# Kernel optimization log

Hardware: AMD Instinct MI355X
Metric: run time of the kernel (lower is better)

The kernel has to match this reference:

```python
import jax, jax.numpy as jnp
import numpy as np

B, N, IN_DIM, D, H, L = 8, 256, 2, 128, 512, 2
EPS = 1e-5


def layer_norm(x, g, b):
    m = jnp.mean(x, axis=-1, keepdims=True)
    v = jnp.var(x, axis=-1, keepdims=True)
    return (x - m) * jax.lax.rsqrt(v + EPS) * g + b


def loo_max_pool(nodes):
    # nodes: (B, N, D) -> leave-one-out max over the set axis -> (B, N, D)
    n = nodes.shape[1]
    neg = jnp.finfo(nodes.dtype).min
    mask = jnp.eye(n, dtype=bool)[None, :, :, None]          # (1, N, N, 1)
    expanded = jnp.broadcast_to(nodes[:, None, :, :],
                                (nodes.shape[0], n, n, nodes.shape[2]))
    return jnp.where(mask, neg, expanded).max(axis=2)        # (B, N, D)


def setup_inputs() -> dict:
    key = jax.random.key(0)
    ks = jax.random.split(key, 16)
    s = 0.02
    inp = {
        "x":   jax.random.normal(ks[0], (B, N, IN_DIM), dtype=jnp.float32),
        # embedding linear + its LayerNorm
        "We":  jax.random.normal(ks[1], (IN_DIM, D)) * s,
        "be":  jnp.zeros((D,), jnp.float32),
        "ge":  jnp.ones((D,), jnp.float32),
        "bge": jnp.zeros((D,), jnp.float32),
        # per-layer pool linear (concat of x and LOO-pooled context: 2D -> D)
        "Wp":  jax.random.normal(ks[2], (L, 2 * D, D)) * s,
        "bp":  jnp.zeros((L, D), jnp.float32),
        "gp":  jnp.ones((L, D), jnp.float32),
        "bgp": jnp.zeros((L, D), jnp.float32),
        # per-layer feed-forward D -> H -> D
        "W1":  jax.random.normal(ks[3], (L, D, H)) * s,
        "b1":  jnp.zeros((L, H), jnp.float32),
        "W2":  jax.random.normal(ks[4], (L, H, D)) * s,
        "b2":  jnp.zeros((L, D), jnp.float32),
        "gf":  jnp.ones((L, D), jnp.float32),
        "bgf": jnp.zeros((L, D), jnp.float32),
    }
    return inp


def reference(x, We, be, ge, bge, Wp, bp, gp, bgp, W1, b1, W2, b2, gf, bgf):
    # embeddings + embedding norm
    h = layer_norm(x @ We + be, ge, bge)                      # (B, N, D)
    for i in range(L):
        # pool layer: LOO max pooling, concat, linear, residual, norm
        pooled = loo_max_pool(h)                              # (B, N, D)
        cat = jnp.concatenate([h, pooled], axis=-1)           # (B, N, 2D)
        h = layer_norm(h + cat @ Wp[i] + bp[i], gp[i], bgp[i])
        # feed-forward, residual, norm
        ff = jax.nn.relu(h @ W1[i] + b1[i]) @ W2[i] + b2[i]
        h = layer_norm(h + ff, gf[i], bgf[i])
    return h
```

## Files before the change

kernel.cpp:

```cpp
#include <hip/hip_runtime.h>
#include <hip/hip_bf16.h>

#define BB 8
#define NN 256
#define DD 128
#define HH 512
#define LL 2
#define EPSV 1e-5f
#define TPB 8
#define BPL (NN/TPB)

typedef unsigned short ushort_t;
typedef __attribute__((ext_vector_type(8))) short bf16x8;
typedef __attribute__((ext_vector_type(4))) float f32x4;

#define WPSZ (256*128)
#define W1SZ (128*512)
#define W2SZ (512*128)
#define LAYSZ (WPSZ+W1SZ+W2SZ)
#define TOTW (2*LAYSZ)

#if defined(__has_builtin)
#if __has_builtin(__builtin_amdgcn_sched_barrier)
#define SCHED_FENCE() __builtin_amdgcn_sched_barrier(0)
#endif
#endif
#ifndef SCHED_FENCE
#define SCHED_FENCE()
#endif

__device__ __forceinline__ ushort_t f2b(float v){
  __hip_bfloat16 h = __float2bfloat16(v);
  return *(ushort_t*)&h;
}

__device__ __forceinline__ void waveRed2(float &a, float &b){
  #pragma unroll
  for (int off=32; off>=1; off>>=1){
    a += __shfl_xor(a, off, 64);
    b += __shfl_xor(b, off, 64);
  }
}

__device__ __forceinline__ void poolMerge(float &m1, float &m2, int &am,
                                          float o1, float o2, int oa){
  if (o1 > m1){ m2 = fmaxf(m1, o2); m1 = o1; am = oa; }
  else        { m2 = fmaxf(m2, o1); }
}

__global__ __launch_bounds__(512) void k_prep(
    const float* __restrict__ Wp, const float* __restrict__ W1,
    const float* __restrict__ W2, ushort_t* __restrict__ wcvt)
{
  int e8 = blockIdx.x*512 + threadIdx.x;
  if (e8 >= TOTW/8) return;
  int e = e8*8;
  int l2 = (e >= LAYSZ) ? 1 : 0;
  int el = e - l2*LAYSZ;
  const float* src; int N, KSlog, off;
  if (el < WPSZ)           { src = Wp + (size_t)l2*WPSZ; N = 128; KSlog = 3; off = el; }
  else if (el < WPSZ+W1SZ) { src = W1 + (size_t)l2*W1SZ; N = 512; KSlog = 2; off = el - WPSZ; }
  else                     { src = W2 + (size_t)l2*W2SZ; N = 128; KSlog = 4; off = el - (WPSZ+W1SZ); }
  int rec  = off >> 9;
  int ln   = (off >> 3) & 63;
  int n0t  = rec >> KSlog;
  int ks   = rec & ((1<<KSlog)-1);
  int row0 = ks*32 + ((ln>>4)<<3);
  int col  = (n0t<<4) + (ln&15);
  bf16x8 v;
  #pragma unroll
  for (int j=0;j<8;++j) v[j] = (short)f2b(src[(size_t)(row0+j)*N + col]);
  *(bf16x8*)(wcvt + e) = v;
}

__global__ __launch_bounds__(512, 2) void k_net(
    int layer,
    const float* __restrict__ x, const float* __restrict__ We,
    const float* __restrict__ be, const float* __restrict__ ge,
    const float* __restrict__ bge,
    float* __restrict__ hio,
    float* __restrict__ pm1, float* __restrict__ pm2, int* __restrict__ pma,
    const ushort_t* __restrict__ wL,
    const float* __restrict__ bp,
    const float* __restrict__ gp, const float* __restrict__ bgp,
    const float* __restrict__ b1,
    const float* __restrict__ b2,
    const float* __restrict__ gf, const float* __restrict__ bgf)
{
  int tid = threadIdx.x;
  int d = tid & 127, fourth = tid >> 7;
  int wv = tid >> 6;
  int lane = tid & 63;
  int m = lane & 15, q = lane >> 4;
  int t0 = blockIdx.x * TPB;
  int b = t0 >> 8;
  int blk = (t0 >> 3) & (BPL-1);
  int n0a = wv*16;

  const ushort_t* wAb = wL;
  const ushort_t* wBb = wL + WPSZ;
  const ushort_t* wCb = wL + WPSZ + W1SZ;

  bf16x8 wfa[8], wfb[16];
  #pragma unroll
  for (int ks=0; ks<8; ++ks)
    wfa[ks] = *(const bf16x8*)(wAb + ((size_t)(wv*8+ks)*64 + lane)*8);
  #pragma unroll
  for (int r=0; r<16; ++r)
    wfb[r] = *(const bf16x8*)(wBb + ((size_t)(((r>>2)*8+wv)*4 + (r&3))*64 + lane)*8);
  SCHED_FENCE();

  __shared__ float    hcur[8*128];
  __shared__ ushort_t catb[16*256];
  __shared__ float    sA[16*128];
  __shared__ ushort_t h1b[16*128];
  __shared__ float    h1f[8*128];
  __shared__ ushort_t ub[16*512];
  __shared__ float fm1[128], fm2[128];
  __shared__ int   fam[128];
  __shared__ float sm1[4][128], sm2[4][128];
  __shared__ int   sam[4][128];
  __shared__ float xs[512];
  __shared__ float red9[2][12];
  __shared__ float stats[12];
  __shared__ float4 tk[256];

  if (layer == 0){
    xs[tid] = x[(size_t)b*512 + tid];
    float a = We[d], bw = We[128+d], c = be[d];
    if (fourth == 0){
      float r0=a, r1=bw;        waveRed2(r0,r1);
      float r2=c, r3=a*a;       waveRed2(r2,r3);
      float r4=bw*bw, r5=c*c;   waveRed2(r4,r5);
      float r6=a*bw, r7=a*c;    waveRed2(r6,r7);
      float r8=bw*c, r9=0.f;    waveRed2(r8,r9);
      int w = (tid >> 6) & 1;
      if (lane == 0){
        red9[w][0]=r0; red9[w][1]=r1; red9[w][2]=r2; red9[w][3]=r3;
        red9[w][4]=r4; red9[w][5]=r5; red9[w][6]=r6; red9[w][7]=r7;
        red9[w][8]=r8;
      }
    }
    __syncthreads();
    if (tid < 9) stats[tid] = (red9[0][tid] + red9[1][tid]) * (1.f/128);
    __syncthreads();
    if (tid < 256){
      float mA=stats[0], mB=stats[1], mC=stats[2];
      float SAA=stats[3], SBB=stats[4], SCC=stats[5];
      float SAB=stats[6], SAC=stats[7], SBC=stats[8];
      float x0 = xs[2*tid], x1 = xs[2*tid+1];
      float mean = fmaf(x0, mA, fmaf(x1, mB, mC));
      float ev2  = x0*x0*SAA + x1*x1*SBB + SCC
                 + 2.f*(x0*x1*SAB + x0*SAC + x1*SBC);
      float var = ev2 - mean*mean;
      tk[tid] = make_float4(x0, x1, mean, rsqrtf(var + EPSV));
    }
    __syncthreads();
    float gev = ge[d], bgev = bge[d];
    float m1=-3.4e38f, m2=-3.4e38f; int am=0;
    for (int i=0;i<64;++i){
      int n = fourth*64 + i;
      float4 t4 = tk[n];
      float v  = fmaf(t4.x, a, fmaf(t4.y, bw, c));
      float hv = fmaf((v - t4.z)*t4.w, gev, bgev);
      poolMerge(m1,m2,am, hv, -3.4e38f, n);
    }
    sm1[fourth][d]=m1; sm2[fourth][d]=m2; sam[fourth][d]=am;
    #pragma unroll
    for (int rep=0; rep<2; ++rep){
      int t = fourth*2 + rep;
      int n = (t0 & 255) + t;
      float4 t4 = tk[n];
      float v  = fmaf(t4.x, a, fmaf(t4.y, bw, c));
      float hv = fmaf((v - t4.z)*t4.w, gev, bgev);
      hcur[t*128 + d] = hv;
      *(ushort_t*)((char*)catb + (((t*256 + d)*2) ^ ((t&7)<<4))) = f2b(hv);
    }
    __syncthreads();
  } else {
    {
      size_t base = ((size_t)b*BPL + fourth*8)*128 + d;
      float m1 = pm1[base], m2 = pm2[base]; int am = pma[base];
      #pragma unroll
      for (int i=1;i<8;++i)
        poolMerge(m1,m2,am, pm1[base+(size_t)i*128], pm2[base+(size_t)i*128],
                  pma[base+(size_t)i*128]);
      sm1[fourth][d]=m1; sm2[fourth][d]=m2; sam[fourth][d]=am;
    }
    #pragma unroll
    for (int rep=0; rep<2; ++rep){
      int t = fourth*2 + rep;
      float hv = hio[(size_t)(t0+t)*DD + d];
      hcur[t*128 + d] = hv;
      *(ushort_t*)((char*)catb + (((t*256 + d)*2) ^ ((t&7)<<4))) = f2b(hv);
    }
    __syncthreads();
  }

  if (fourth==0){
    float m1=sm1[0][d], m2=sm2[0][d]; int am=sam[0][d];
    #pragma unroll
    for (int p=1;p<4;++p) poolMerge(m1,m2,am, sm1[p][d], sm2[p][d], sam[p][d]);
    fm1[d]=m1; fm2[d]=m2; fam[d]=am;
  }
  __syncthreads();

  #pragma unroll
  for (int rep=0; rep<2; ++rep){
    int e = rep*512 + tid;
    int t = e >> 7, c2 = e & 127;
    int n = (t0 & 255) + t;
    float v = (n==fam[c2]) ? fm2[c2] : fm1[c2];
    *(ushort_t*)((char*)catb + (((t*256 + 128 + c2)*2) ^ ((t&7)<<4))) = f2b(v);
  }
  __syncthreads();

  {
    f32x4 acc = {0.f,0.f,0.f,0.f};
    const char* apb = (const char*)catb;
    int abase = (m*256 + q*8)*2;
    int sw = (m&7)<<4;
    #pragma unroll
    for (int ks=0; ks<8; ++ks){
      bf16x8 af = *(const bf16x8*)(apb + ((abase + ks*64) ^ sw));
      acc = __builtin_amdgcn_mfma_f32_16x16x32_bf16(af, wfa[ks], acc, 0,0,0);
    }
    #pragma unroll
    for (int r=0;r<4;++r) sA[(q*4+r)*128 + n0a + m] = acc[r];
  }
  bf16x8 wfc[16];
  #pragma unroll
  for (int kk=0; kk<16; ++kk)
    wfc[kk] = *(const bf16x8*)(wCb + ((size_t)(wv*16+kk)*64 + lane)*8);
  SCHED_FENCE();
  __syncthreads();

  {
    int t = wv, g = lane;
    float2 v2 = *(const float2*)&sA[t*128 + 2*g];
    float v0 = v2.x + bp[2*g]   + hcur[t*128 + 2*g];
    float v1 = v2.y + bp[2*g+1] + hcur[t*128 + 2*g + 1];
    float s = v0+v1, qq = v0*v0 + v1*v1;
    waveRed2(s,qq);
    float mean = s*(1.f/128), var = qq*(1.f/128) - mean*mean;
    float rs = rsqrtf(var + EPSV);
    float o0 = (v0-mean)*rs*gp[2*g]   + bgp[2*g];
    float o1 = (v1-mean)*rs*gp[2*g+1] + bgp[2*g+1];
    unsigned pk = (unsigned)f2b(o0) | ((unsigned)f2b(o1) << 16);
    *(unsigned*)((char*)h1b + (((t*128 + 2*g)*2) ^ ((t&7)<<4))) = pk;
    *(float2*)&h1f[t*128 + 2*g] = make_float2(o0, o1);
  }
  __syncthreads();

  {
    const char* apb = (const char*)h1b;
    int abase = (m*128 + q*8)*2;
    int sw = (m&7)<<4;
    bf16x8 af[4];
    #pragma unroll
    for (int ks=0; ks<4; ++ks)
      af[ks] = *(const bf16x8*)(apb + ((abase + ks*64) ^ sw));
    #pragma unroll
    for (int half=0; half<2; ++half){
      #pragma unroll
      for (int i=0;i<2;++i){
        int idx4 = half*2+i;
        int n0 = idx4*128 + wv*16;
        f32x4 acc = {0.f,0.f,0.f,0.f};
        #pragma unroll
        for (int ks=0; ks<4; ++ks)
          acc = __builtin_amdgcn_mfma_f32_16x16x32_bf16(af[ks], wfb[idx4*4+ks], acc, 0,0,0);
        float bb = b1[n0+m];
        #pragma unroll
        for (int r=0;r<4;++r){
          int row = q*4+r;
          *(ushort_t*)((char*)ub + (((row*512 + n0 + m)*2) ^ ((row&7)<<4)))
              = f2b(fmaxf(acc[r] + bb, 0.f));
        }
      }
    }
  }
  __syncthreads();

  {
    f32x4 acc = {0.f,0.f,0.f,0.f};
    const char* apb = (const char*)ub;
    int abase = (m*512 + q*8)*2;
    int sw = (m&7)<<4;
    #pragma unroll
    for (int kk=0; kk<16; ++kk){
      bf16x8 af = *(const bf16x8*)(apb + ((abase + kk*64) ^ sw));
      acc = __builtin_amdgcn_mfma_f32_16x16x32_bf16(af, wfc[kk], acc, 0,0,0);
    }
    #pragma unroll
    for (int r=0;r<4;++r) sA[(q*4+r)*128 + n0a + m] = acc[r];
  }
  __syncthreads();

  {
    int t = wv, g = lane;
    float2 v2 = *(const float2*)&sA[t*128 + 2*g];
    float v0 = v2.x + b2[2*g]   + h1f[t*128 + 2*g];
    float v1 = v2.y + b2[2*g+1] + h1f[t*128 + 2*g + 1];
    float s = v0+v1, qq = v0*v0 + v1*v1;
    waveRed2(s,qq);
    float mean = s*(1.f/128), var = qq*(1.f/128) - mean*mean;
    float rs = rsqrtf(var + EPSV);
    float o0 = (v0-mean)*rs*gf[2*g]   + bgf[2*g];
    float o1 = (v1-mean)*rs*gf[2*g+1] + bgf[2*g+1];
    *(float2*)&hio[(size_t)(t0+t)*DD + 2*g] = make_float2(o0, o1);
    *(float2*)&hcur[t*128 + 2*g] = make_float2(o0, o1);
  }
  if (layer == 0){
    __syncthreads();
    if (tid < 128){
      int n0 = t0 & 255;
      float m1 = hcur[tid], m2 = -3.4e38f; int am = n0;
      #pragma unroll
      for (int p=1;p<TPB;++p)
        poolMerge(m1,m2,am, hcur[p*128+tid], -3.4e38f, n0+p);
      size_t idx = ((size_t)b*BPL + blk)*128 + tid;
      pm1[idx]=m1; pm2[idx]=m2; pma[idx]=am;
    }
  }
}

extern "C" void kernel_launch(void* const* d_in, const int* in_sizes, int n_in,
                              void* d_out, int out_size, void* d_ws, size_t ws_size,
                              hipStream_t stream)
{
  const float* x   = (const float*)d_in[0];
  const float* We  = (const float*)d_in[1];
  const float* be  = (const float*)d_in[2];
  const float* ge  = (const float*)d_in[3];
  const float* bge = (const float*)d_in[4];
  const float* Wp  = (const float*)d_in[5];
  const float* bp  = (const float*)d_in[6];
  const float* gp  = (const float*)d_in[7];
  const float* bgp = (const float*)d_in[8];
  const float* W1  = (const float*)d_in[9];
  const float* b1  = (const float*)d_in[10];
  const float* W2  = (const float*)d_in[11];
  const float* b2  = (const float*)d_in[12];
  const float* gf  = (const float*)d_in[13];
  const float* bgf = (const float*)d_in[14];

  float* hio = (float*)d_out;
  char* ws = (char*)d_ws;
  const size_t NP = (size_t)BB*BPL*128;
  float* p1 = (float*)ws;            ws += NP*4;
  float* p2 = (float*)ws;            ws += NP*4;
  int*   pa = (int*)ws;              ws += NP*4;
  ushort_t* wcvt = (ushort_t*)ws;

  const int grid = (BB*NN)/TPB;

  k_prep<<<80, 512, 0, stream>>>(Wp, W1, W2, wcvt);

  k_net<<<grid, 512, 0, stream>>>(0, x, We, be, ge, bge, hio, p1, p2, pa,
      wcvt,
      bp,      gp,      bgp,
      b1,      b2,
      gf,      bgf);

  k_net<<<grid, 512, 0, stream>>>(1, x, We, be, ge, bge, hio, p1, p2, pa,
      wcvt + LAYSZ,
      bp + DD, gp + DD, bgp + DD,
      b1 + HH, b2 + DD,
      gf + DD, bgf + DD);
}
```

Baseline: 103.6 us.

## Hoist embedding LayerNorm and pooled max stats into prep kernel

Before this change, each of the 256 layer-0 blocks recomputed the embedding LayerNorm for all 256 set elements of its batch so it could find the leave-one-out max statistics. Now 8 extra blocks in the prep kernel compute h0 and the per-batch top-2 and argmax once, and write them to workspace. Layer-0 blocks just read their rows and the stats. This removes redundant per-block compute and shared memory, at the cost of a global round trip for h0 (1 MB) and a serial dependency on the prep kernel.

```diff
diff --git a/kernel.cpp b/kernel.cpp
--- a/kernel.cpp
+++ b/kernel.cpp
@@ -19,6 +19,7 @@
 #define W2SZ (512*128)
 #define LAYSZ (WPSZ+W1SZ+W2SZ)
 #define TOTW (2*LAYSZ)
+#define WBLK 80
 
 #if defined(__has_builtin)
 #if __has_builtin(__builtin_amdgcn_sched_barrier)
@@ -50,37 +51,104 @@
 
 __global__ __launch_bounds__(512) void k_prep(
     const float* __restrict__ Wp, const float* __restrict__ W1,
-    const float* __restrict__ W2, ushort_t* __restrict__ wcvt)
-{
-  int e8 = blockIdx.x*512 + threadIdx.x;
-  if (e8 >= TOTW/8) return;
-  int e = e8*8;
-  int l2 = (e >= LAYSZ) ? 1 : 0;
-  int el = e - l2*LAYSZ;
-  const float* src; int N, KSlog, off;
-  if (el < WPSZ)           { src = Wp + (size_t)l2*WPSZ; N = 128; KSlog = 3; off = el; }
-  else if (el < WPSZ+W1SZ) { src = W1 + (size_t)l2*W1SZ; N = 512; KSlog = 2; off = el - WPSZ; }
-  else                     { src = W2 + (size_t)l2*W2SZ; N = 128; KSlog = 4; off = el - (WPSZ+W1SZ); }
-  int rec  = off >> 9;
-  int ln   = (off >> 3) & 63;
-  int n0t  = rec >> KSlog;
-  int ks   = rec & ((1<<KSlog)-1);
-  int row0 = ks*32 + ((ln>>4)<<3);
-  int col  = (n0t<<4) + (ln&15);
-  bf16x8 v;
-  #pragma unroll
-  for (int j=0;j<8;++j) v[j] = (short)f2b(src[(size_t)(row0+j)*N + col]);
-  *(bf16x8*)(wcvt + e) = v;
-}
-
-__global__ __launch_bounds__(512, 2) void k_net(
-    int layer,
+    const float* __restrict__ W2,
     const float* __restrict__ x, const float* __restrict__ We,
     const float* __restrict__ be, const float* __restrict__ ge,
     const float* __restrict__ bge,
+    ushort_t* __restrict__ wcvt, float* __restrict__ h0w,
+    float* __restrict__ fm1w, float* __restrict__ fm2w,
+    int* __restrict__ famw)
+{
+  int tid = threadIdx.x;
+  if (blockIdx.x < WBLK){
+    int e8 = blockIdx.x*512 + tid;
+    int e = e8*8;
+    int l2 = (e >= LAYSZ) ? 1 : 0;
+    int el = e - l2*LAYSZ;
+    const float* src; int N, KSlog, off;
+    if (el < WPSZ)           { src = Wp + (size_t)l2*WPSZ; N = 128; KSlog = 3; off = el; }
+    else if (el < WPSZ+W1SZ) { src = W1 + (size_t)l2*W1SZ; N = 512; KSlog = 2; off = el - WPSZ; }
+    else                     { src = W2 + (size_t)l2*W2SZ; N = 128; KSlog = 4; off = el - (WPSZ+W1SZ); }
+    int rec  = off >> 9;
+    int ln   = (off >> 3) & 63;
+    int n0t  = rec >> KSlog;
+    int ks   = rec & ((1<<KSlog)-1);
+    int row0 = ks*32 + ((ln>>4)<<3);
+    int col  = (n0t<<4) + (ln&15);
+    bf16x8 v;
+    #pragma unroll
+    for (int j=0;j<8;++j) v[j] = (short)f2b(src[(size_t)(row0+j)*N + col]);
+    *(bf16x8*)(wcvt + e) = v;
+    return;
+  }
+
+  int bb = blockIdx.x - WBLK;
+  int d = tid & 127, fourth = tid >> 7, lane = tid & 63;
+
+  __shared__ float xs[512];
+  __shared__ float red9[2][12];
+  __shared__ float stats[12];
+  __shared__ float4 tk[256];
+  __shared__ float sm1[4][128], sm2[4][128];
+  __shared__ int   sam[4][128];
+
+  xs[tid] = x[(size_t)bb*512 + tid];
+  float a = We[d], bw = We[128+d], c = be[d];
+  if (fourth == 0){
+    float r0=a, r1=bw;        waveRed2(r0,r1);
+    float r2=c, r3=a*a;       waveRed2(r2,r3);
+    float r4=bw*bw, r5=c*c;   waveRed2(r4,r5);
+    float r6=a*bw, r7=a*c;    waveRed2(r6,r7);
+    float r8=bw*c, r9=0.f;    waveRed2(r8,r9);
+    int w = (tid >> 6) & 1;
+    if (lane == 0){
+      red9[w][0]=r0; red9[w][1]=r1; red9[w][2]=r2; red9[w][3]=r3;
+      red9[w][4]=r4; red9[w][5]=r5; red9[w][6]=r6; red9[w][7]=r7;
+      red9[w][8]=r8;
+    }
+  }
+  __syncthreads();
+  if (tid < 9) stats[tid] = (red9[0][tid] + red9[1][tid]) * (1.f/128);
+  __syncthreads();
+  if (tid < 256){
+    float mA=stats[0], mB=stats[1], mC=stats[2];
+    float SAA=stats[3], SBB=stats[4], SCC=stats[5];
+    float SAB=stats[6], SAC=stats[7], SBC=stats[8];
+    float x0 = xs[2*tid], x1 = xs[2*tid+1];
+    float mean = fmaf(x0, mA, fmaf(x1, mB, mC));
+    float ev2  = x0*x0*SAA + x1*x1*SBB + SCC
+               + 2.f*(x0*x1*SAB + x0*SAC + x1*SBC);
+    float var = ev2 - mean*mean;
+    tk[tid] = make_float4(x0, x1, mean, rsqrtf(var + EPSV));
+  }
+  __syncthreads();
+  float gev = ge[d], bgev = bge[d];
+  float m1=-3.4e38f, m2=-3.4e38f; int am=0;
+  for (int i=0;i<64;++i){
+    int n = fourth*64 + i;
+    float4 t4 = tk[n];
+    float v  = fmaf(t4.x, a, fmaf(t4.y, bw, c));
+    float hv = fmaf((v - t4.z)*t4.w, gev, bgev);
+    h0w[((size_t)bb*256 + n)*128 + d] = hv;
+    poolMerge(m1,m2,am, hv, -3.4e38f, n);
+  }
+  sm1[fourth][d]=m1; sm2[fourth][d]=m2; sam[fourth][d]=am;
+  __syncthreads();
+  if (fourth==0){
+    float M1=sm1[0][d], M2=sm2[0][d]; int AM=sam[0][d];
+    #pragma unroll
+    for (int p=1;p<4;++p) poolMerge(M1,M2,AM, sm1[p][d], sm2[p][d], sam[p][d]);
+    fm1w[bb*128+d]=M1; fm2w[bb*128+d]=M2; famw[bb*128+d]=AM;
+  }
+}
+
+__global__ __launch_bounds__(512, 2) void k_net(
+    int layer,
     float* __restrict__ hio,
     float* __restrict__ pm1, float* __restrict__ pm2, int* __restrict__ pma,
     const ushort_t* __restrict__ wL,
+    const float* __restrict__ h0w, const float* __restrict__ fm1w,
+    const float* __restrict__ fm2w, const int* __restrict__ famw,
     const float* __restrict__ bp,
     const float* __restrict__ gp, const float* __restrict__ bgp,
     const float* __restrict__ b1,
@@ -120,61 +188,28 @@
   __shared__ int   fam[128];
   __shared__ float sm1[4][128], sm2[4][128];
   __shared__ int   sam[4][128];
-  __shared__ float xs[512];
-  __shared__ float red9[2][12];
-  __shared__ float stats[12];
-  __shared__ float4 tk[256];
 
   if (layer == 0){
-    xs[tid] = x[(size_t)b*512 + tid];
-    float a = We[d], bw = We[128+d], c = be[d];
-    if (fourth == 0){
-      float r0=a, r1=bw;        waveRed2(r0,r1);
-      float r2=c, r3=a*a;       waveRed2(r2,r3);
-      float r4=bw*bw, r5=c*c;   waveRed2(r4,r5);
-      float r6=a*bw, r7=a*c;    waveRed2(r6,r7);
-      float r8=bw*c, r9=0.f;    waveRed2(r8,r9);
-      int w = (tid >> 6) & 1;
-      if (lane == 0){
-        red9[w][0]=r0; red9[w][1]=r1; red9[w][2]=r2; red9[w][3]=r3;
-        red9[w][4]=r4; red9[w][5]=r5; red9[w][6]=r6; red9[w][7]=r7;
-        red9[w][8]=r8;
-      }
-    }
-    __syncthreads();
-    if (tid < 9) stats[tid] = (red9[0][tid] + red9[1][tid]) * (1.f/128);
-    __syncthreads();
-    if (tid < 256){
-      float mA=stats[0], mB=stats[1], mC=stats[2];
-      float SAA=stats[3], SBB=stats[4], SCC=stats[5];
-      float SAB=stats[6], SAC=stats[7], SBC=stats[8];
-      float x0 = xs[2*tid], x1 = xs[2*tid+1];
-      float mean = fmaf(x0, mA, fmaf(x1, mB, mC));
-      float ev2  = x0*x0*SAA + x1*x1*SBB + SCC
-                 + 2.f*(x0*x1*SAB + x0*SAC + x1*SBC);
-      float var = ev2 - mean*mean;
-      tk[tid] = make_float4(x0, x1, mean, rsqrtf(var + EPSV));
-    }
-    __syncthreads();
-    float gev = ge[d], bgev = bge[d];
-    float m1=-3.4e38f, m2=-3.4e38f; int am=0;
-    for (int i=0;i<64;++i){
-      int n = fourth*64 + i;
-      float4 t4 = tk[n];
-      float v  = fmaf(t4.x, a, fmaf(t4.y, bw, c));
-      float hv = fmaf((v - t4.z)*t4.w, gev, bgev);
-      poolMerge(m1,m2,am, hv, -3.4e38f, n);
-    }
-    sm1[fourth][d]=m1; sm2[fourth][d]=m2; sam[fourth][d]=am;
     #pragma unroll
     for (int rep=0; rep<2; ++rep){
       int t = fourth*2 + rep;
-      int n = (t0 & 255) + t;
-      float4 t4 = tk[n];
-      float v  = fmaf(t4.x, a, fmaf(t4.y, bw, c));
-      float hv = fmaf((v - t4.z)*t4.w, gev, bgev);
+      float hv = h0w[(size_t)(t0+t)*DD + d];
       hcur[t*128 + d] = hv;
       *(ushort_t*)((char*)catb + (((t*256 + d)*2) ^ ((t&7)<<4))) = f2b(hv);
+    }
+    {
+      int c2 = tid & 127;
+      float f1  = fm1w[b*128 + c2];
+      float f2v = fm2w[b*128 + c2];
+      int   fa  = famw[b*128 + c2];
+      #pragma unroll
+      for (int rep=0; rep<2; ++rep){
+        int e = rep*512 + tid;
+        int t = e >> 7;
+        int n = (t0 & 255) + t;
+        float v = (n==fa) ? f2v : f1;
+        *(ushort_t*)((char*)catb + (((t*256 + 128 + c2)*2) ^ ((t&7)<<4))) = f2b(v);
+      }
     }
     __syncthreads();
   } else {
@@ -195,25 +230,23 @@
       *(ushort_t*)((char*)catb + (((t*256 + d)*2) ^ ((t&7)<<4))) = f2b(hv);
     }
     __syncthreads();
-  }
-
-  if (fourth==0){
-    float m1=sm1[0][d], m2=sm2[0][d]; int am=sam[0][d];
-    #pragma unroll
-    for (int p=1;p<4;++p) poolMerge(m1,m2,am, sm1[p][d], sm2[p][d], sam[p][d]);
-    fm1[d]=m1; fm2[d]=m2; fam[d]=am;
-  }
-  __syncthreads();
-
-  #pragma unroll
-  for (int rep=0; rep<2; ++rep){
-    int e = rep*512 + tid;
-    int t = e >> 7, c2 = e & 127;
-    int n = (t0 & 255) + t;
-    float v = (n==fam[c2]) ? fm2[c2] : fm1[c2];
-    *(ushort_t*)((char*)catb + (((t*256 + 128 + c2)*2) ^ ((t&7)<<4))) = f2b(v);
-  }
-  __syncthreads();
+    if (fourth==0){
+      float m1=sm1[0][d], m2=sm2[0][d]; int am=sam[0][d];
+      #pragma unroll
+      for (int p=1;p<4;++p) poolMerge(m1,m2,am, sm1[p][d], sm2[p][d], sam[p][d]);
+      fm1[d]=m1; fm2[d]=m2; fam[d]=am;
+    }
+    __syncthreads();
+    #pragma unroll
+    for (int rep=0; rep<2; ++rep){
+      int e = rep*512 + tid;
+      int t = e >> 7, c2 = e & 127;
+      int n = (t0 & 255) + t;
+      float v = (n==fam[c2]) ? fm2[c2] : fm1[c2];
+      *(ushort_t*)((char*)catb + (((t*256 + 128 + c2)*2) ^ ((t&7)<<4))) = f2b(v);
+    }
+    __syncthreads();
+  }
 
   {
     f32x4 acc = {0.f,0.f,0.f,0.f};
@@ -351,20 +384,25 @@
   float* p1 = (float*)ws;            ws += NP*4;
   float* p2 = (float*)ws;            ws += NP*4;
   int*   pa = (int*)ws;              ws += NP*4;
-  ushort_t* wcvt = (ushort_t*)ws;
+  ushort_t* wcvt = (ushort_t*)ws;    ws += (size_t)TOTW*2;
+  float* h0w  = (float*)ws;          ws += (size_t)BB*NN*DD*4;
+  float* fm1w = (float*)ws;          ws += (size_t)BB*128*4;
+  float* fm2w = (float*)ws;          ws += (size_t)BB*128*4;
+  int*   famw = (int*)ws;            ws += (size_t)BB*128*4;
 
   const int grid = (BB*NN)/TPB;
 
-  k_prep<<<80, 512, 0, stream>>>(Wp, W1, W2, wcvt);
-
-  k_net<<<grid, 512, 0, stream>>>(0, x, We, be, ge, bge, hio, p1, p2, pa,
-      wcvt,
+  k_prep<<<WBLK + BB, 512, 0, stream>>>(Wp, W1, W2, x, We, be, ge, bge,
+                                        wcvt, h0w, fm1w, fm2w, famw);
+
+  k_net<<<grid, 512, 0, stream>>>(0, hio, p1, p2, pa,
+      wcvt, h0w, fm1w, fm2w, famw,
       bp,      gp,      bgp,
       b1,      b2,
       gf,      bgf);
 
-  k_net<<<grid, 512, 0, stream>>>(1, x, We, be, ge, bge, hio, p1, p2, pa,
-      wcvt + LAYSZ,
+  k_net<<<grid, 512, 0, stream>>>(1, hio, p1, p2, pa,
+      wcvt + LAYSZ, h0w, fm1w, fm2w, famw,
       bp + DD, gp + DD, bgp + DD,
       b1 + HH, b2 + DD,
       gf + DD, bgf + DD);
```

Result: no change. 104.5 us (+0.9%).
